# Performance work log

Measured on AMD Instinct MI355X. Metric: run time of the kernel, lower is better.

## Reference

```python
import jax, jax.numpy as jnp
from jax import lax
import numpy as np

EPS = 0.1          # DBSCAN radius (init arg eps)
MIN_SAMPLES = 5    # DBSCAN min_samples (init arg min_samples)
NC_MAX = 512       # fixed padded cluster budget (8 per dim * 64 dims)


def _dbscan_1d(x):
    """Exact 1-D DBSCAN on a vector x of shape (N,).
    Returns (labels, n_clusters). labels[i] in [-1, n_clusters), -1 = noise.
    Clusters are numbered in ascending value order (canonical deterministic
    relabeling of sklearn's discovery order). Border points are attached to
    the nearest core point (ties -> left)."""
    n = x.shape[0]
    order = jnp.argsort(x)
    xs = x[order]
    # core test: #points within [xs-eps, xs+eps] >= min_samples
    hi = jnp.searchsorted(xs, xs + EPS, side='right')
    lo = jnp.searchsorted(xs, xs - EPS, side='left')
    core = (hi - lo) >= MIN_SAMPLES
    inf = jnp.inf
    core_vals = jnp.where(core, xs, -inf)
    run_max = lax.cummax(core_vals, axis=0)                 # nearest core value to the left (incl self)
    prev_core_val = jnp.concatenate([jnp.full((1,), -inf, xs.dtype), run_max[:-1]])
    # a core point starts a new cluster iff no core point within eps on its left
    new_cluster = core & ((xs - prev_core_val) > EPS)
    starts = jnp.cumsum(new_cluster.astype(jnp.int32))
    cid = starts - 1                                        # cluster id carried along sorted order
    ncl = starts[-1]
    # nearest core on the left / right (values and their cluster ids)
    left_cid = lax.cummax(jnp.where(core, cid, -1), axis=0)
    left_val = run_max
    right_cid = lax.cummin(jnp.where(core, cid, n + 1), axis=0, reverse=True)
    right_val = lax.cummin(jnp.where(core, xs, inf), axis=0, reverse=True)
    dl = xs - left_val
    dr = right_val - xs
    border_cid = jnp.where(dl <= dr, left_cid, right_cid)
    border_ok = jnp.minimum(dl, dr) <= EPS
    lab_sorted = jnp.where(core, cid, jnp.where(border_ok, border_cid, -1))
    labels = jnp.zeros_like(lab_sorted).at[order].set(lab_sorted)  # unsort to original node order
    return labels, ncl


def setup_inputs() -> dict:
    key = jax.random.key(0)
    features = jax.random.normal(key, (8, 16384, 64), dtype=jnp.float32)
    return {"features": features}


def reference(features):
    B, N, D = features.shape
    xt = jnp.transpose(features, (0, 2, 1))                  # (B, D, N)
    labels, ncl = jax.vmap(jax.vmap(_dbscan_1d))(xt)         # (B, D, N), (B, D)
    off = jnp.cumsum(ncl, axis=1) - ncl                      # exclusive prefix: global cluster offset per dim
    glb = jnp.where(labels >= 0, labels + off[:, :, None], -1)
    # noise / overflow -> dump into padding column NC_MAX, sliced off below
    lbl = jnp.where(glb >= 0, jnp.minimum(glb, NC_MAX), NC_MAX)
    inc = jnp.zeros((B, N, NC_MAX + 1), features.dtype)
    b_ix = jnp.arange(B)[:, None, None]
    n_ix = jnp.arange(N)[None, None, :]
    inc = inc.at[b_ix, n_ix, lbl].set(1.0)                   # scatter cluster membership
    return inc[:, :, :NC_MAX]                                # (B, N, NC_MAX) padded incidence matrix
```

## Files before the change

### kernel.cpp

```cpp
#include <hip/hip_runtime.h>

#define NPTS   16384
#define NDIM   64
#define NBATCH 8
#define TB     1024
#define VPT    16
#define NB     8192
#define BPT    8
#define EPSF   0.1f
#define MINS   5
#define NCMAX  512
#define BIGI   0x3fffffff

typedef short short8 __attribute__((ext_vector_type(8)));
typedef float f32x4  __attribute__((ext_vector_type(4)));

__device__ __forceinline__ int phys(int i)  { return i ^ ((i >> 5) & 15); }
__device__ __forceinline__ int lphys(int i) { return i ^ (((i >> 6) & 31) << 1); }

__device__ __forceinline__ int binof(float x, float mn, float inv) {
  float fb = (x - mn) * inv;
  int b = (int)fb;
  if (fb < 0.f) b = 0;
  if (b > NB - 1) b = NB - 1;
  return b;
}

__global__ void ktrans(const float* __restrict__ f, float* __restrict__ xt) {
  __shared__ float tile[64][65];
  int blk = blockIdx.x;
  int b   = blk >> 8;
  int n0  = (blk & 255) << 6;
  for (int i = threadIdx.x; i < 64 * 64; i += 256) {
    int n = i >> 6, d = i & 63;
    tile[n][d] = f[((size_t)b * NPTS + n0 + n) * NDIM + d];
  }
  __syncthreads();
  for (int i = threadIdx.x; i < 64 * 64; i += 256) {
    int d = i >> 6, n = i & 63;
    xt[((size_t)b * NDIM + d) * NPTS + n0 + n] = tile[n][d];
  }
}

struct FS { int h; float f; float l; int c; };
__device__ __forceinline__ FS fsid() { FS r; r.h = 0; r.f = 0.f; r.l = 0.f; r.c = 0; return r; }
__device__ __forceinline__ FS fscomb(FS a, FS b) {
  FS r;
  r.h = a.h | b.h;
  r.f = a.h ? a.f : b.f;
  r.l = b.h ? b.l : a.l;
  int gap = (a.h && b.h && ((b.f - a.l) > EPSF)) ? 1 : 0;
  r.c = a.c + b.c + gap;
  return r;
}

__global__ void __launch_bounds__(TB) kdbscan(const float* __restrict__ xt,
                                              short* __restrict__ labels,
                                              int* __restrict__ nclg) {
  const int tid  = threadIdx.x;
  const int lane = tid & 63;
  const int wid  = tid >> 6;
  const int bd   = blockIdx.x;
  const float* __restrict__ x = xt + (size_t)bd * NPTS;

  __shared__ float xs[NPTS];
  __shared__ unsigned int hist[NB];
  __shared__ unsigned int offs[NB + 1];
  __shared__ float wmn[16], wmx[16];
  __shared__ unsigned int wsum[16];
  __shared__ int   sh[16];  __shared__ float sf[16], sl[16]; __shared__ int sc[16];
  __shared__ int   wri[16]; __shared__ float wrv[16];
  short* lab = (short*)hist;

  float v[VPT];
  float mn = INFINITY, mx = -INFINITY;
  #pragma unroll
  for (int s = 0; s < VPT; ++s) {
    v[s] = x[tid + s * TB];
    mn = fminf(mn, v[s]); mx = fmaxf(mx, v[s]);
  }
  for (int d = 1; d < 64; d <<= 1) {
    mn = fminf(mn, __shfl_xor(mn, d));
    mx = fmaxf(mx, __shfl_xor(mx, d));
  }
  if (lane == 0) { wmn[wid] = mn; wmx[wid] = mx; }
  __syncthreads();
  mn = wmn[0]; mx = wmx[0];
  for (int w = 1; w < 16; ++w) { mn = fminf(mn, wmn[w]); mx = fmaxf(mx, wmx[w]); }
  float range = mx - mn;
  float inv = (range > 0.f) ? ((float)NB / range) : 0.f;

  for (int i = tid; i < NB; i += TB) hist[i] = 0u;
  __syncthreads();
  #pragma unroll
  for (int s = 0; s < VPT; ++s) atomicAdd(&hist[binof(v[s], mn, inv)], 1u);
  __syncthreads();

  unsigned int loc[BPT];
  unsigned int run = 0;
  const int bbase = tid * BPT;
  #pragma unroll
  for (int j = 0; j < BPT; ++j) { loc[j] = run; run += hist[bbase + j]; }
  unsigned int incl = run;
  for (int d = 1; d < 64; d <<= 1) {
    unsigned int u = __shfl_up(incl, d);
    if (lane >= d) incl += u;
  }
  unsigned int exc = __shfl_up(incl, 1);
  if (lane == 0) exc = 0u;
  if (lane == 63) wsum[wid] = incl;
  __syncthreads();
  unsigned int wb = 0;
  for (int w = 0; w < wid; ++w) wb += wsum[w];
  unsigned int tb0 = wb + exc;
  #pragma unroll
  for (int j = 0; j < BPT; ++j) offs[bbase + j] = tb0 + loc[j];
  if (tid == TB - 1) offs[NB] = NPTS;
  __syncthreads();

  int pos[VPT];
  #pragma unroll
  for (int s = 0; s < VPT; ++s) {
    int b = binof(v[s], mn, inv);
    unsigned old = atomicSub(&hist[b], 1u);
    int p = (int)(offs[b] + old - 1u);
    pos[s] = p | (b << 14);
    xs[phys(p)] = v[s];
  }
  __syncthreads();

  int tgt[VPT];
  #pragma unroll
  for (int s = 0; s < VPT; ++s) {
    int b  = pos[s] >> 14;
    int pp = pos[s] & 0x3FFF;
    int s0 = (int)offs[b];
    int e0 = (int)offs[b + 1];
    float vv = v[s];
    int r = 0;
    for (int j = s0; j < e0; ++j) {
      float xj = xs[phys(j)];
      r += (xj < vv || (xj == vv && j < pp)) ? 1 : 0;
    }
    tgt[s] = s0 + r;
  }
  __syncthreads();

  #pragma unroll
  for (int s = 0; s < VPT; ++s) xs[phys(tgt[s])] = v[s];
  __syncthreads();

  const int p0 = tid * VPT;
  float w[VPT + 8];
  #pragma unroll
  for (int k = 0; k < VPT + 8; ++k) {
    int i = p0 - 4 + k;
    w[k] = (i < 0) ? -INFINITY : ((i >= NPTS) ? INFINITY : xs[phys(i)]);
  }
  unsigned int coremask = 0u;
  FS ch = fsid();
  int fi = BIGI; float fv = 0.f;
  #pragma unroll
  for (int s = 0; s < VPT; ++s) {
    float xi = w[s + 4];
    float lo = xi - EPSF, hi = xi + EPSF;
    bool core = false;
    #pragma unroll
    for (int t = 0; t < MINS; ++t)
      core |= (w[s + 4 - t] >= lo) && (w[s + 8 - t] <= hi);
    if (core) {
      coremask |= (1u << s);
      if (!ch.h) { ch.h = 1; ch.f = xi; }
      else if ((xi - ch.l) > EPSF) ++ch.c;
      ch.l = xi;
      if (fi == BIGI) { fi = p0 + s; fv = xi; }
    }
  }

  FS cur = ch;
  for (int d = 1; d < 64; d <<= 1) {
    FS u;
    u.h = __shfl_up(cur.h, d);
    u.f = __shfl_up(cur.f, d);
    u.l = __shfl_up(cur.l, d);
    u.c = __shfl_up(cur.c, d);
    FS cmb = fscomb(u, cur);
    if (lane >= d) cur = cmb;
  }
  FS exs;
  exs.h = __shfl_up(cur.h, 1);
  exs.f = __shfl_up(cur.f, 1);
  exs.l = __shfl_up(cur.l, 1);
  exs.c = __shfl_up(cur.c, 1);
  if (lane == 0) exs = fsid();
  if (lane == 63) { sh[wid] = cur.h; sf[wid] = cur.f; sl[wid] = cur.l; sc[wid] = cur.c; }
  __syncthreads();
  FS pre = fsid();
  for (int w2 = 0; w2 < wid; ++w2) {
    FS t; t.h = sh[w2]; t.f = sf[w2]; t.l = sl[w2]; t.c = sc[w2];
    pre = fscomb(pre, t);
  }
  FS sp = fscomb(pre, exs);

  int ri = fi; float rv = fv;
  for (int d = 1; d < 64; d <<= 1) {
    int ui = __shfl_down(ri, d); float uv = __shfl_down(rv, d);
    if (lane < 64 - d && ui < ri) { ri = ui; rv = uv; }
  }
  int Ri = __shfl_down(ri, 1); float Rv = __shfl_down(rv, 1);
  if (lane == 63) Ri = BIGI;
  if (lane == 0) { wri[wid] = ri; wrv[wid] = rv; }
  __syncthreads();
  for (int w2 = wid + 1; w2 < 16; ++w2)
    if (wri[w2] < Ri) { Ri = wri[w2]; Rv = wrv[w2]; }

  float P  = sp.h ? sp.l : -INFINITY;
  int starts = sp.h ? (sp.c + 1) : 0;
  #pragma unroll
  for (int s = 0; s < VPT; ++s) {
    int i = p0 + s;
    float xi = w[s + 4];
    short lb;
    if ((coremask >> s) & 1u) {
      if ((xi - P) > EPSF) ++starts;
      P = xi;
      lb = (short)(starts - 1);
    } else {
      float dl = xi - P;
      unsigned hb = coremask >> (s + 1);
      float Rv2; bool has;
      if (hb) { int j = s + 1 + __builtin_ctz(hb); Rv2 = w[4 + j]; has = true; }
      else    { Rv2 = Rv; has = (Ri < NPTS); }
      float dr = has ? (Rv2 - xi) : INFINITY;
      lb = -1;
      if (fminf(dl, dr) <= EPSF)
        lb = (short)((dl <= dr) ? (starts - 1)
                                : (starts - 1 + (((Rv2 - P) > EPSF) ? 1 : 0)));
    }
    lab[lphys(i)] = lb;
  }
  if (tid == TB - 1) nclg[bd] = starts;
  __syncthreads();

  #pragma unroll
  for (int s = 0; s < VPT; ++s)
    labels[(size_t)bd * NPTS + tid + s * TB] = lab[lphys(tgt[s])];
}

__global__ void __launch_bounds__(TB) kout(const short* __restrict__ labels,
                                           const int* __restrict__ ncl,
                                           float* __restrict__ out) {
  const int tid  = threadIdx.x;
  const int lane = tid & 63;
  const int wid  = tid >> 6;
  const int b    = blockIdx.x >> 5;
  const int n0   = (blockIdx.x & 31) * 512 + wid * 32;

  __shared__ int cmLDS[NCMAX];
  for (int k = tid; k < NCMAX; k += TB) cmLDS[k] = -1;
  __syncthreads();
  if (tid < 64) {
    int vcnt = ncl[b * 64 + tid];
    int incl = vcnt;
    for (int d = 1; d < 64; d <<= 1) {
      int u = __shfl_up(incl, d);
      if (tid >= d) incl += u;
    }
    int off = incl - vcnt;
    for (int k = 0; k < vcnt; ++k) {
      int col = off + k;
      if (col < NCMAX) cmLDS[col] = tid | (k << 8);
    }
  }
  __syncthreads();

  int dk[8], kk[8];
  #pragma unroll
  for (int k = 0; k < 8; ++k) {
    int col = (k < 4) ? (lane * 4 + k) : (256 + lane * 4 + (k - 4));
    int m = cmLDS[col];
    dk[k] = (m >= 0) ? (m & 255) : 0;
    kk[k] = (m >= 0) ? (m >> 8) : 0x7FFF;
  }
  const short* lb_b = labels + (size_t)b * NDIM * NPTS;

  #pragma unroll
  for (int rc = 0; rc < 4; ++rc) {
    short8 L[8];
    #pragma unroll
    for (int k = 0; k < 8; ++k)
      L[k] = *(const short8*)(lb_b + (size_t)dk[k] * NPTS + n0 + rc * 8);
    #pragma unroll
    for (int r2 = 0; r2 < 8; ++r2) {
      int n = n0 + rc * 8 + r2;
      float o[8];
      #pragma unroll
      for (int k = 0; k < 8; ++k)
        o[k] = (L[k][r2] == (short)kk[k]) ? 1.0f : 0.0f;
      f32x4* op = (f32x4*)(out + ((size_t)b * NPTS + n) * NCMAX);
      f32x4 lo4 = { o[0], o[1], o[2], o[3] };
      f32x4 hi4 = { o[4], o[5], o[6], o[7] };
      __builtin_nontemporal_store(lo4, &op[lane]);
      __builtin_nontemporal_store(hi4, &op[64 + lane]);
    }
  }
}

extern "C" void kernel_launch(void* const* d_in, const int* in_sizes, int n_in,
                              void* d_out, int out_size, void* d_ws, size_t ws_size,
                              hipStream_t stream) {
  const float* feat = (const float*)d_in[0];
  float* out = (float*)d_out;

  char* ws = (char*)d_ws;
  size_t xt_b   = (size_t)NBATCH * NPTS * NDIM * 4;
  size_t lbl_b  = (size_t)NBATCH * NPTS * NDIM * 2;
  float* xt     = (float*)ws;
  short* labels = (short*)(ws + xt_b);
  int*   ncl    = (int*)(ws + xt_b + lbl_b);

  ktrans  <<<NBATCH * (NPTS / 64), 256, 0, stream>>>(feat, xt);
  kdbscan <<<NBATCH * NDIM, TB, 0, stream>>>(xt, labels, ncl);
  kout    <<<NBATCH * 32, TB, 0, stream>>>(labels, ncl, out);
}
```

Baseline: 152.7 us.

## Alias LDS buffers in DBSCAN kernel to cut shared memory footprint

Reuses the sorted-value buffer for the histogram and label storage, and compresses bin offsets to 16-bit, shrinking shared memory per block substantially. The scatter into the sorted buffer is split into a separate pass after the histogram atomics, with extra barriers to keep the aliasing safe. The intent is to allow more than one 1024-thread block resident per CU, so the per-dimension blocks run in fewer waves. It adds barriers and an extra pass over registers in exchange.

```diff
diff --git a/kernel.cpp b/kernel.cpp
--- a/kernel.cpp
+++ b/kernel.cpp
@@ -16,7 +16,6 @@
 typedef float f32x4  __attribute__((ext_vector_type(4)));
 
 __device__ __forceinline__ int phys(int i)  { return i ^ ((i >> 5) & 15); }
-__device__ __forceinline__ int lphys(int i) { return i ^ (((i >> 6) & 31) << 1); }
 
 __device__ __forceinline__ int binof(float x, float mn, float inv) {
   float fb = (x - mn) * inv;
@@ -64,13 +63,18 @@
   const float* __restrict__ x = xt + (size_t)bd * NPTS;
 
   __shared__ float xs[NPTS];
-  __shared__ unsigned int hist[NB];
-  __shared__ unsigned int offs[NB + 1];
-  __shared__ float wmn[16], wmx[16];
-  __shared__ unsigned int wsum[16];
-  __shared__ int   sh[16];  __shared__ float sf[16], sl[16]; __shared__ int sc[16];
-  __shared__ int   wri[16]; __shared__ float wrv[16];
-  short* lab = (short*)hist;
+  __shared__ unsigned short offsw[NB];
+  unsigned* hist = (unsigned*)xs;
+  int*      labi = (int*)xs;
+  float*    wmn  = (float*)offsw;
+  float*    wmx  = (float*)offsw + 16;
+  unsigned* wsum = (unsigned*)offsw;
+  int*      sh   = (int*)offsw;
+  float*    sf   = (float*)offsw + 16;
+  float*    sl   = (float*)offsw + 32;
+  int*      sc   = (int*)offsw + 48;
+  int*      wri  = (int*)offsw + 64;
+  float*    wrv  = (float*)offsw + 80;
 
   float v[VPT];
   float mn = INFINITY, mx = -INFINITY;
@@ -89,6 +93,7 @@
   for (int w = 1; w < 16; ++w) { mn = fminf(mn, wmn[w]); mx = fmaxf(mx, wmx[w]); }
   float range = mx - mn;
   float inv = (range > 0.f) ? ((float)NB / range) : 0.f;
+  __syncthreads();
 
   for (int i = tid; i < NB; i += TB) hist[i] = 0u;
   __syncthreads();
@@ -113,9 +118,9 @@
   unsigned int wb = 0;
   for (int w = 0; w < wid; ++w) wb += wsum[w];
   unsigned int tb0 = wb + exc;
-  #pragma unroll
-  for (int j = 0; j < BPT; ++j) offs[bbase + j] = tb0 + loc[j];
-  if (tid == TB - 1) offs[NB] = NPTS;
+  __syncthreads();
+  #pragma unroll
+  for (int j = 0; j < BPT; ++j) offsw[bbase + j] = (unsigned short)(tb0 + loc[j]);
   __syncthreads();
 
   int pos[VPT];
@@ -123,10 +128,13 @@
   for (int s = 0; s < VPT; ++s) {
     int b = binof(v[s], mn, inv);
     unsigned old = atomicSub(&hist[b], 1u);
-    int p = (int)(offs[b] + old - 1u);
+    int p = (int)offsw[b] + (int)old - 1;
     pos[s] = p | (b << 14);
-    xs[phys(p)] = v[s];
-  }
+  }
+  __syncthreads();
+
+  #pragma unroll
+  for (int s = 0; s < VPT; ++s) xs[phys(pos[s] & 0x3FFF)] = v[s];
   __syncthreads();
 
   int tgt[VPT];
@@ -134,8 +142,8 @@
   for (int s = 0; s < VPT; ++s) {
     int b  = pos[s] >> 14;
     int pp = pos[s] & 0x3FFF;
-    int s0 = (int)offs[b];
-    int e0 = (int)offs[b + 1];
+    int s0 = (int)offsw[b];
+    int e0 = (b < NB - 1) ? (int)offsw[b + 1] : NPTS;
     float vv = v[s];
     int r = 0;
     for (int j = s0; j < e0; ++j) {
@@ -220,11 +228,11 @@
   for (int s = 0; s < VPT; ++s) {
     int i = p0 + s;
     float xi = w[s + 4];
-    short lb;
+    int lb;
     if ((coremask >> s) & 1u) {
       if ((xi - P) > EPSF) ++starts;
       P = xi;
-      lb = (short)(starts - 1);
+      lb = starts - 1;
     } else {
       float dl = xi - P;
       unsigned hb = coremask >> (s + 1);
@@ -234,17 +242,17 @@
       float dr = has ? (Rv2 - xi) : INFINITY;
       lb = -1;
       if (fminf(dl, dr) <= EPSF)
-        lb = (short)((dl <= dr) ? (starts - 1)
-                                : (starts - 1 + (((Rv2 - P) > EPSF) ? 1 : 0)));
-    }
-    lab[lphys(i)] = lb;
+        lb = (dl <= dr) ? (starts - 1)
+                        : (starts - 1 + (((Rv2 - P) > EPSF) ? 1 : 0));
+    }
+    labi[phys(i)] = lb;
   }
   if (tid == TB - 1) nclg[bd] = starts;
   __syncthreads();
 
   #pragma unroll
   for (int s = 0; s < VPT; ++s)
-    labels[(size_t)bd * NPTS + tid + s * TB] = lab[lphys(tgt[s])];
+    labels[(size_t)bd * NPTS + tid + s * TB] = (short)labi[phys(tgt[s])];
 }
 
 __global__ void __launch_bounds__(TB) kout(const short* __restrict__ labels,
```

After: 153.6 us. No clear change (+0.6%).

## Compute per-dimension min/max in transpose kernel and merge block barriers

Applied to the files above, without the earlier changes.

The transpose kernel now also reduces per-(batch,dim) min and max, using order-preserving float-to-uint flips and shared then global atomics. kdbscan reads these values instead of doing its own block-wide min/max reduction, which removes one barrier and a shuffle reduction. It also moves the right-nearest-core shuffle scan ahead of the shared barrier so two __syncthreads merge into one. The cost is two extra memset launches and global atomics in ktrans.

```diff
diff --git a/kernel.cpp b/kernel.cpp
--- a/kernel.cpp
+++ b/kernel.cpp
@@ -26,20 +26,40 @@
   return b;
 }
 
-__global__ void ktrans(const float* __restrict__ f, float* __restrict__ xt) {
+__device__ __forceinline__ unsigned flipf(float x) {
+  unsigned u = __float_as_uint(x);
+  return (u & 0x80000000u) ? ~u : (u | 0x80000000u);
+}
+__device__ __forceinline__ float unflipf(unsigned y) {
+  return __uint_as_float((y & 0x80000000u) ? (y & 0x7FFFFFFFu) : ~y);
+}
+
+__global__ void ktrans(const float* __restrict__ f, float* __restrict__ xt,
+                       unsigned* __restrict__ mng, unsigned* __restrict__ mxg) {
   __shared__ float tile[64][65];
+  __shared__ unsigned smn[64], smx[64];
+  const int tid = threadIdx.x;
   int blk = blockIdx.x;
   int b   = blk >> 8;
   int n0  = (blk & 255) << 6;
-  for (int i = threadIdx.x; i < 64 * 64; i += 256) {
+  if (tid < 64) { smn[tid] = 0xFFFFFFFFu; smx[tid] = 0u; }
+  float lmn = INFINITY, lmx = -INFINITY;
+  for (int i = tid; i < 64 * 64; i += 256) {
     int n = i >> 6, d = i & 63;
-    tile[n][d] = f[((size_t)b * NPTS + n0 + n) * NDIM + d];
-  }
-  __syncthreads();
-  for (int i = threadIdx.x; i < 64 * 64; i += 256) {
+    float t = f[((size_t)b * NPTS + n0 + n) * NDIM + d];
+    tile[n][d] = t;
+    lmn = fminf(lmn, t); lmx = fmaxf(lmx, t);
+  }
+  __syncthreads();
+  atomicMin(&smn[tid & 63], flipf(lmn));
+  atomicMax(&smx[tid & 63], flipf(lmx));
+  __syncthreads();
+  for (int i = tid; i < 64 * 64; i += 256) {
     int d = i >> 6, n = i & 63;
     xt[((size_t)b * NDIM + d) * NPTS + n0 + n] = tile[n][d];
   }
+  if (tid < 64)       atomicMin(&mng[b * 64 + tid], smn[tid]);
+  else if (tid < 128) atomicMax(&mxg[b * 64 + (tid - 64)], smx[tid - 64]);
 }
 
 struct FS { int h; float f; float l; int c; };
@@ -55,6 +75,8 @@
 }
 
 __global__ void __launch_bounds__(TB) kdbscan(const float* __restrict__ xt,
+                                              const unsigned* __restrict__ mng,
+                                              const unsigned* __restrict__ mxg,
                                               short* __restrict__ labels,
                                               int* __restrict__ nclg) {
   const int tid  = threadIdx.x;
@@ -66,32 +88,21 @@
   __shared__ float xs[NPTS];
   __shared__ unsigned int hist[NB];
   __shared__ unsigned int offs[NB + 1];
-  __shared__ float wmn[16], wmx[16];
   __shared__ unsigned int wsum[16];
   __shared__ int   sh[16];  __shared__ float sf[16], sl[16]; __shared__ int sc[16];
   __shared__ int   wri[16]; __shared__ float wrv[16];
   short* lab = (short*)hist;
 
-  float v[VPT];
-  float mn = INFINITY, mx = -INFINITY;
-  #pragma unroll
-  for (int s = 0; s < VPT; ++s) {
-    v[s] = x[tid + s * TB];
-    mn = fminf(mn, v[s]); mx = fmaxf(mx, v[s]);
-  }
-  for (int d = 1; d < 64; d <<= 1) {
-    mn = fminf(mn, __shfl_xor(mn, d));
-    mx = fmaxf(mx, __shfl_xor(mx, d));
-  }
-  if (lane == 0) { wmn[wid] = mn; wmx[wid] = mx; }
-  __syncthreads();
-  mn = wmn[0]; mx = wmx[0];
-  for (int w = 1; w < 16; ++w) { mn = fminf(mn, wmn[w]); mx = fmaxf(mx, wmx[w]); }
+  float mn = unflipf(mng[bd]);
+  float mx = unflipf(mxg[bd]);
   float range = mx - mn;
   float inv = (range > 0.f) ? ((float)NB / range) : 0.f;
-
   for (int i = tid; i < NB; i += TB) hist[i] = 0u;
-  __syncthreads();
+  float v[VPT];
+  #pragma unroll
+  for (int s = 0; s < VPT; ++s) v[s] = x[tid + s * TB];
+  __syncthreads();
+
   #pragma unroll
   for (int s = 0; s < VPT; ++s) atomicAdd(&hist[binof(v[s], mn, inv)], 1u);
   __syncthreads();
@@ -193,24 +204,25 @@
   exs.l = __shfl_up(cur.l, 1);
   exs.c = __shfl_up(cur.c, 1);
   if (lane == 0) exs = fsid();
+
+  int ri = fi; float rv = fv;
+  for (int d = 1; d < 64; d <<= 1) {
+    int ui = __shfl_down(ri, d); float uv = __shfl_down(rv, d);
+    if (lane < 64 - d && ui < ri) { ri = ui; rv = uv; }
+  }
+  int Ri = __shfl_down(ri, 1); float Rv = __shfl_down(rv, 1);
+  if (lane == 63) Ri = BIGI;
+
   if (lane == 63) { sh[wid] = cur.h; sf[wid] = cur.f; sl[wid] = cur.l; sc[wid] = cur.c; }
-  __syncthreads();
+  if (lane == 0)  { wri[wid] = ri;  wrv[wid] = rv; }
+  __syncthreads();
+
   FS pre = fsid();
   for (int w2 = 0; w2 < wid; ++w2) {
     FS t; t.h = sh[w2]; t.f = sf[w2]; t.l = sl[w2]; t.c = sc[w2];
     pre = fscomb(pre, t);
   }
   FS sp = fscomb(pre, exs);
-
-  int ri = fi; float rv = fv;
-  for (int d = 1; d < 64; d <<= 1) {
-    int ui = __shfl_down(ri, d); float uv = __shfl_down(rv, d);
-    if (lane < 64 - d && ui < ri) { ri = ui; rv = uv; }
-  }
-  int Ri = __shfl_down(ri, 1); float Rv = __shfl_down(rv, 1);
-  if (lane == 63) Ri = BIGI;
-  if (lane == 0) { wri[wid] = ri; wrv[wid] = rv; }
-  __syncthreads();
   for (int w2 = wid + 1; w2 < 16; ++w2)
     if (wri[w2] < Ri) { Ri = wri[w2]; Rv = wrv[w2]; }
 
@@ -318,8 +330,12 @@
   float* xt     = (float*)ws;
   short* labels = (short*)(ws + xt_b);
   int*   ncl    = (int*)(ws + xt_b + lbl_b);
-
-  ktrans  <<<NBATCH * (NPTS / 64), 256, 0, stream>>>(feat, xt);
-  kdbscan <<<NBATCH * NDIM, TB, 0, stream>>>(xt, labels, ncl);
+  unsigned* mng = (unsigned*)(ncl + NBATCH * NDIM);
+  unsigned* mxg = mng + NBATCH * NDIM;
+
+  hipMemsetAsync(mng, 0xFF, NBATCH * NDIM * sizeof(unsigned), stream);
+  hipMemsetAsync(mxg, 0x00, NBATCH * NDIM * sizeof(unsigned), stream);
+  ktrans  <<<NBATCH * (NPTS / 64), 256, 0, stream>>>(feat, xt, mng, mxg);
+  kdbscan <<<NBATCH * NDIM, TB, 0, stream>>>(xt, mng, mxg, labels, ncl);
   kout    <<<NBATCH * 32, TB, 0, stream>>>(labels, ncl, out);
 }
```

After: 163.6 us. 7.1% more time.
